# Kernel optimization log

Measured on AMD Instinct MI355X. Metric: run time of the kernel, lower is better.

Reference implementation:

```python
import jax, jax.numpy as jnp
import numpy as np
from jax import lax

# Hyperparameters from init_kwargs (inference/testing path of the RPN)
PRE_NMS = 6000        # pre_nms_top_n['testing']
POST_NMS = 1000       # post_nms_top_n['testing']
NMS_THRESH = 0.7
MIN_SIZE = 1.0
WX = WY = WW = WH = 1.0                      # reg_weights
BBOX_XFORM_CLIP = float(np.log(1000.0 / 16.0))  # standard BoxCoder clamp on dw/dh


def _decode(deltas, anchors):
    # deltas, anchors: [K, 4] -> decoded boxes [K, 4] (x1,y1,x2,y2)
    wa = anchors[:, 2] - anchors[:, 0]
    ha = anchors[:, 3] - anchors[:, 1]
    cxa = anchors[:, 0] + 0.5 * wa
    cya = anchors[:, 1] + 0.5 * ha
    dx = deltas[:, 0] / WX
    dy = deltas[:, 1] / WY
    dw = jnp.minimum(deltas[:, 2] / WW, BBOX_XFORM_CLIP)
    dh = jnp.minimum(deltas[:, 3] / WH, BBOX_XFORM_CLIP)
    cx = dx * wa + cxa
    cy = dy * ha + cya
    w = jnp.exp(dw) * wa
    h = jnp.exp(dh) * ha
    return jnp.stack([cx - 0.5 * w, cy - 0.5 * h, cx + 0.5 * w, cy + 0.5 * h], axis=-1)


def _nms_keep(boxes, valid, thresh):
    # Sequential NMS over score-sorted boxes [K,4]; 'valid' marks non-removed boxes.
    K = boxes.shape[0]
    x1, y1, x2, y2 = boxes[:, 0], boxes[:, 1], boxes[:, 2], boxes[:, 3]
    areas = (x2 - x1) * (y2 - y1)
    idxs = jnp.arange(K)

    def body(i, keep):
        xx1 = jnp.maximum(x1[i], x1)
        yy1 = jnp.maximum(y1[i], y1)
        xx2 = jnp.minimum(x2[i], x2)
        yy2 = jnp.minimum(y2[i], y2)
        inter = jnp.maximum(xx2 - xx1, 0.0) * jnp.maximum(yy2 - yy1, 0.0)
        iou = inter / (areas[i] + areas - inter + 1e-9)
        suppress = (iou > thresh) & (idxs > i)
        return jnp.where(keep[i], keep & ~suppress, keep)

    return lax.fori_loop(0, K, body, valid)


def _proposals_one(anchors, objectness, deltas, img_h, img_w):
    # anchors [N,4], objectness [N], deltas [N,4] -> proposals [POST_NMS, 4]
    k = min(objectness.shape[0], PRE_NMS)
    scores, idx = lax.top_k(objectness, k)          # topk filter (sorted desc)
    boxes = _decode(deltas[idx], anchors[idx])      # anchor decode on top-k only
    # process_box: clip to image, filter small boxes (masked, not removed, for jit)
    x1 = jnp.clip(boxes[:, 0], 0.0, img_w)
    y1 = jnp.clip(boxes[:, 1], 0.0, img_h)
    x2 = jnp.clip(boxes[:, 2], 0.0, img_w)
    y2 = jnp.clip(boxes[:, 3], 0.0, img_h)
    boxes = jnp.stack([x1, y1, x2, y2], axis=-1)
    valid = ((x2 - x1) >= MIN_SIZE) & ((y2 - y1) >= MIN_SIZE)
    keep = _nms_keep(boxes, valid, NMS_THRESH)
    # Compact kept boxes (score order) into a fixed [POST_NMS,4] buffer, zero-padded
    rank = jnp.cumsum(keep.astype(jnp.int32)) - 1
    tgt = jnp.where(keep & (rank < POST_NMS), rank, POST_NMS)  # POST_NMS -> dropped
    out = jnp.zeros((POST_NMS, 4), boxes.dtype).at[tgt].set(boxes, mode='drop')
    return out


def setup_inputs() -> dict:
    key = jax.random.key(0)
    k1, k2, k3, k4 = jax.random.split(key, 4)
    B, N = 8, 500000
    IMG = 1024
    # Valid anchor boxes: random centers in-image, sizes in [16, 256]
    cxy = jax.random.uniform(k1, (B, N, 2), jnp.float32, 0.0, float(IMG))
    wh = jax.random.uniform(k2, (B, N, 2), jnp.float32, 16.0, 256.0)
    anchors = jnp.concatenate([cxy - 0.5 * wh, cxy + 0.5 * wh], axis=-1)
    objectness = jax.random.normal(k3, (B, N), jnp.float32)
    pred_bbox_delta = 0.1 * jax.random.normal(k4, (B, N, 4), jnp.float32)
    return {"anchors": anchors, "objectness": objectness,
            "pred_bbox_delta": pred_bbox_delta, "img_h": IMG, "img_w": IMG}


def reference(anchors, objectness, pred_bbox_delta, img_h, img_w):
    h, w = float(img_h), float(img_w)
    f = jax.vmap(lambda a, o, d: _proposals_one(a, o, d, h, w))
    return f(anchors, objectness, pred_bbox_delta)  # [B, POST_NMS, 4]
```

## Files before the change

### kernel.cpp

```cpp
#include <hip/hip_runtime.h>
#include <cstdint>
#include <cmath>

#define NBATCH   8
#define NPB      500000
#define PRE_NMS  6000
#define POST_NMS 1000
#define NWORDS   94
#define NBINS    16384
#define CANDCAP  8192
#define BBOX_CLIP 4.135166556742356f
#define TI 16
#define TJ 512
#define WIN 16
#define CNT_PAD 64
#define SORT_CHUNK 2048

#define F_SORT 1u
#define F_COMP 2u
#define F_OOB  4u

__device__ __forceinline__ unsigned monot(float f) {
    unsigned b = __float_as_uint(f);
    return (b & 0x80000000u) ? ~b : (b | 0x80000000u);
}

__device__ __forceinline__ bool iou_gt_thr(float inter, float den) {
    const double MID = (double)0.7f + 0x1p-25;
    return (double)inter >= MID * (double)den;
}

__global__ __launch_bounds__(256) void hist_kernel(const float* __restrict__ obj,
                                                   unsigned* __restrict__ hist) {
    __shared__ unsigned lh[NBINS];
    const int b = blockIdx.y;
    for (int q = threadIdx.x; q < NBINS; q += 256) lh[q] = 0;
    __syncthreads();
    const float* p = obj + (size_t)b * NPB;
    const int stride = gridDim.x * 256;
    for (int i = blockIdx.x * 256 + threadIdx.x; i < NPB; i += stride) {
        unsigned u = monot(p[i]);
        atomicAdd(&lh[u >> 18], 1u);
    }
    __syncthreads();
    unsigned* gh = hist + (size_t)b * NBINS;
    for (int q = threadIdx.x; q < NBINS; q += 256) {
        unsigned v = lh[q];
        if (v) atomicAdd(&gh[q], v);
    }
}

__global__ __launch_bounds__(256) void thresh_kernel(const unsigned* __restrict__ hist,
                                                     unsigned* __restrict__ tbin) {
    __shared__ unsigned part[256], pre[256];
    const int b = blockIdx.x;
    const unsigned* gh = hist + (size_t)b * NBINS;
    const int t = threadIdx.x;
    const int PER = NBINS / 256;
    unsigned s = 0;
    for (int d = 0; d < PER; ++d) s += gh[NBINS - 1 - (t * PER + d)];
    part[t] = s;
    __syncthreads();
    if (t == 0) {
        unsigned run = 0;
        for (int q = 0; q < 256; ++q) { pre[q] = run; run += part[q]; }
    }
    __syncthreads();
    unsigned c = pre[t];
    if (c < PRE_NMS && c + part[t] >= PRE_NMS) {
        unsigned run = c;
        for (int d = 0; d < PER; ++d) {
            int bin = NBINS - 1 - (t * PER + d);
            run += gh[bin];
            if (run >= PRE_NMS) { tbin[b] = (unsigned)bin; break; }
        }
    }
}

__global__ __launch_bounds__(256) void compact_kernel(const float* __restrict__ obj,
                                                      const unsigned* __restrict__ tbin,
                                                      unsigned long long* __restrict__ cand,
                                                      unsigned* __restrict__ ccnt) {
    const int b = blockIdx.y;
    const unsigned T = tbin[b];
    const float* p = obj + (size_t)b * NPB;
    unsigned long long* cb = cand + (size_t)b * CANDCAP;
    const int lane = threadIdx.x & 63;
    const int stride = gridDim.x * 256;
    for (int i = blockIdx.x * 256 + threadIdx.x; i < NPB; i += stride) {
        unsigned u = monot(p[i]);
        const bool pred = (u >> 18) >= T;
        unsigned long long bal = __ballot(pred);
        if (bal == 0) continue;
        unsigned base = 0;
        if (lane == 0) base = atomicAdd(&ccnt[(size_t)b * CNT_PAD], __popcll(bal));
        base = (unsigned)__shfl((int)base, 0);
        if (pred) {
            unsigned pos = base + (unsigned)__popcll(bal & ((1ULL << lane) - 1ULL));
            if (pos < CANDCAP)
                cb[pos] = ((unsigned long long)u << 32) | (unsigned)(~i);
        }
    }
}

__global__ __launch_bounds__(512) void sort_local_kernel(unsigned long long* __restrict__ cand) {
    __shared__ unsigned long long s[SORT_CHUNK];
    const int blk = blockIdx.x;
    const int b = blk >> 2, c = blk & 3;
    unsigned long long* cb = cand + (size_t)b * CANDCAP + (size_t)c * SORT_CHUNK;
    const int t = threadIdx.x;
    for (int i = t; i < SORT_CHUNK; i += 512) s[i] = cb[i];
    __syncthreads();
    for (unsigned k = 2; k <= SORT_CHUNK; k <<= 1) {
        const bool kfull = (k == SORT_CHUNK);
        const bool upfull = (c & 1) == 0;
        for (unsigned j = k >> 1; j > 0; j >>= 1) {
            for (unsigned ii = t; ii < SORT_CHUNK; ii += 512) {
                unsigned l = ii ^ j;
                if (l > ii) {
                    unsigned long long a = s[ii], d = s[l];
                    bool up = kfull ? upfull : ((ii & k) == 0);
                    if (up ? (a < d) : (a > d)) { s[ii] = d; s[l] = a; }
                }
            }
            __syncthreads();
        }
    }
    for (int i = t; i < SORT_CHUNK; i += 512) cb[i] = s[i];
}

__global__ __launch_bounds__(1024) void sort_merge_kernel(const unsigned long long* __restrict__ cand,
                                                          const float* __restrict__ obj,
                                                          unsigned* __restrict__ topk,
                                                          unsigned* __restrict__ flags) {
    __shared__ unsigned long long s[CANDCAP];
    const int b = blockIdx.x, t = threadIdx.x;
    const unsigned long long* cb = cand + (size_t)b * CANDCAP;
    for (int i = t; i < CANDCAP; i += 1024) s[i] = cb[i];
    __syncthreads();
    for (unsigned k = 2 * SORT_CHUNK; k <= CANDCAP; k <<= 1) {
        for (unsigned j = k >> 1; j > 0; j >>= 1) {
            for (unsigned ii = t; ii < CANDCAP; ii += 1024) {
                unsigned l = ii ^ j;
                if (l > ii) {
                    unsigned long long a = s[ii], c = s[l];
                    bool up = (ii & k) == 0;
                    if (up ? (a < c) : (a > c)) { s[ii] = c; s[l] = a; }
                }
            }
            __syncthreads();
        }
    }
    unsigned f = 0;
    for (int r = t; r < PRE_NMS; r += 1024) {
        unsigned long long c = s[r];
        unsigned idx = ~(unsigned)(c & 0xffffffffULL);
        if (idx >= NPB) { f |= F_OOB; idx = 0; }
        else if (monot(obj[(size_t)b * NPB + idx]) != (unsigned)(c >> 32)) f |= F_COMP;
        if (r < PRE_NMS - 1 && !(c > s[r + 1])) f |= F_SORT;
        topk[(size_t)b * PRE_NMS + r] = idx;
    }
    if (f) atomicOr(&flags[b], f);
}

__global__ __launch_bounds__(256) void decode_kernel(const float* __restrict__ anchors,
                                                     const float* __restrict__ deltas,
                                                     const unsigned* __restrict__ topk,
                                                     const int* __restrict__ imh,
                                                     const int* __restrict__ imw,
                                                     float* __restrict__ boxes,
                                                     float* __restrict__ areas,
                                                     unsigned long long* __restrict__ validm) {
    const int b = blockIdx.y;
    const int r = blockIdx.x * 256 + threadIdx.x;
    const bool active = r < PRE_NMS;
    int vh = imh[0], vw = imw[0];
    float ih = (vh > 0 && vh < (1 << 20)) ? (float)vh : __int_as_float(vh);
    float iw = (vw > 0 && vw < (1 << 20)) ? (float)vw : __int_as_float(vw);
    bool valid = false;
    if (active) {
        unsigned idx = topk[(size_t)b * PRE_NMS + r];
        if (idx >= NPB) idx = 0;
        const float4 a = ((const float4*)anchors)[(size_t)b * NPB + idx];
        const float4 d = ((const float4*)deltas)[(size_t)b * NPB + idx];
        float wa = a.z - a.x, ha = a.w - a.y;
        float cxa = a.x + 0.5f * wa, cya = a.y + 0.5f * ha;
        float dw = fminf(d.z, BBOX_CLIP), dh = fminf(d.w, BBOX_CLIP);
        float cx = __fadd_rn(__fmul_rn(d.x, wa), cxa);
        float cy = __fadd_rn(__fmul_rn(d.y, ha), cya);
        float ew = (float)::exp((double)dw), eh = (float)::exp((double)dh);
        float w = __fmul_rn(ew, wa), h = __fmul_rn(eh, ha);
        float x1 = cx - 0.5f * w, y1 = cy - 0.5f * h;
        float x2 = cx + 0.5f * w, y2 = cy + 0.5f * h;
        x1 = fminf(fmaxf(x1, 0.f), iw); y1 = fminf(fmaxf(y1, 0.f), ih);
        x2 = fminf(fmaxf(x2, 0.f), iw); y2 = fminf(fmaxf(y2, 0.f), ih);
        valid = (x2 - x1 >= 1.0f) && (y2 - y1 >= 1.0f);
        ((float4*)boxes)[(size_t)b * PRE_NMS + r] = make_float4(x1, y1, x2, y2);
        areas[(size_t)b * PRE_NMS + r] = __fmul_rn(x2 - x1, y2 - y1);
    }
    unsigned long long bal = __ballot(valid);
    int w = r >> 6;
    if ((threadIdx.x & 63) == 0 && w < NWORDS) validm[(size_t)b * NWORDS + w] = bal;
}

__global__ __launch_bounds__(256) void mask_kernel(const float* __restrict__ boxes,
                                                   const float* __restrict__ areas,
                                                   unsigned long long* __restrict__ mask) {
    __shared__ float4 sb[TJ];
    __shared__ float  sa[TJ];
    const int b = blockIdx.x & 7;
    const int i0 = (blockIdx.x >> 3) * TI;
    const int jbase = (i0 >> 6) << 6;
    const int wv = threadIdx.x >> 6, ln = threadIdx.x & 63;
    const int ir = i0 + 4 * wv;
    float4 bx[4]; float ar[4]; int wlo[4];
    unsigned long long* rowp[4];
#pragma unroll
    for (int r = 0; r < 4; ++r) {
        const int i = ir + r;
        bx[r]   = ((const float4*)boxes)[(size_t)b * PRE_NMS + i];
        ar[r]   = areas[(size_t)b * PRE_NMS + i];
        rowp[r] = mask + ((size_t)b * PRE_NMS + i) * NWORDS;
        wlo[r]  = i >> 6;
    }
    for (int t0 = jbase; t0 < NWORDS * 64; t0 += TJ) {
        for (int e = threadIdx.x; e < TJ; e += 256) {
            int j = t0 + e;
            if (j < PRE_NMS) {
                sb[e] = ((const float4*)boxes)[(size_t)b * PRE_NMS + j];
                sa[e] = areas[(size_t)b * PRE_NMS + j];
            } else { sb[e] = make_float4(0.f, 0.f, 0.f, 0.f); sa[e] = 0.f; }
        }
        __syncthreads();
        for (int wl = 0; wl < TJ / 64; ++wl) {
            const int w = (t0 >> 6) + wl;
            if (w >= NWORDS) break;
            const int e = wl * 64 + ln;
            const int j = t0 + e;
            const float4 bj = sb[e];
            const float aj = sa[e];
            const bool jin = (j < PRE_NMS);
#pragma unroll
            for (int r = 0; r < 4; ++r) {
                float xx1 = fmaxf(bx[r].x, bj.x), yy1 = fmaxf(bx[r].y, bj.y);
                float xx2 = fminf(bx[r].z, bj.z), yy2 = fminf(bx[r].w, bj.w);
                float inter = __fmul_rn(fmaxf(__fsub_rn(xx2, xx1), 0.f),
                                        fmaxf(__fsub_rn(yy2, yy1), 0.f));
                float den = __fadd_rn(__fsub_rn(__fadd_rn(ar[r], aj), inter), 1e-9f);
                bool p = jin && (j > ir + r) && iou_gt_thr(inter, den);
                unsigned long long m = __ballot(p);
                if (ln == 0 && w >= wlo[r]) rowp[r][w] = m;
            }
        }
        __syncthreads();
    }
}

__global__ __launch_bounds__(64) void scan_kernel(const unsigned long long* __restrict__ mask,
                                                  const unsigned long long* __restrict__ validm,
                                                  const float* __restrict__ boxes,
                                                  const unsigned* __restrict__ flags,
                                                  const unsigned* __restrict__ ccnt,
                                                  float* __restrict__ out) {
    const int b = blockIdx.x, lane = threadIdx.x;
    const unsigned long long* mb = mask + (size_t)b * PRE_NMS * NWORDS;
    const int w0 = 2 * lane, w1 = 2 * lane + 1;
    unsigned long long r_lo = (w0 < NWORDS) ? ~validm[(size_t)b * NWORDS + w0] : ~0ULL;
    unsigned long long r_hi = (w1 < NWORDS) ? ~validm[(size_t)b * NWORDS + w1] : ~0ULL;
    int count = 0;

    uint4 MA[WIN], MB[WIN], MC[WIN];
    unsigned long long WA[WIN], WB[WIN], WC[WIN];
    float4 bxA, bxB, bxC;

#define ISSUE(M, W, BX, base_)                                                   \
    {                                                                            \
        const int bb_ = (base_);                                                 \
        const char* rb_ = (const char*)(mb + (size_t)bb_ * NWORDS);              \
        const int wI_ = bb_ >> 6;                                                \
        _Pragma("unroll")                                                        \
        for (int q = 0; q < WIN; ++q) {                                          \
            const char* rp_ = rb_ + (size_t)q * (NWORDS * 8);                    \
            M[q] = *(const uint4*)(rp_ + (size_t)lane * 16);                     \
            W[q] = *(const unsigned long long*)(rp_ + (size_t)wI_ * 8);          \
        }                                                                        \
        BX = (lane < WIN)                                                        \
                 ? ((const float4*)boxes)[(size_t)b * PRE_NMS + bb_ + lane]      \
                 : make_float4(0.f, 0.f, 0.f, 0.f);                              \
    }

#define RESOLVE(M, W, BX, base_)                                                 \
    {                                                                            \
        const int bb_ = (base_);                                                 \
        const int wR_ = bb_ >> 6, s0_ = bb_ & 63;                                \
        const unsigned long long sel_ = (wR_ & 1) ? r_hi : r_lo;                 \
        const int srcl_ = wR_ >> 1;                                              \
        const unsigned lo_ = (unsigned)__shfl((int)(unsigned)(sel_ & 0xffffffffULL), srcl_); \
        const unsigned hi_ = (unsigned)__shfl((int)(unsigned)(sel_ >> 32), srcl_);           \
        const unsigned long long ww_ = ((unsigned long long)hi_ << 32) | lo_;    \
        unsigned cand_ = (unsigned)((~ww_) >> s0_) & 0xFFFFu;                    \
        unsigned kept_ = 0;                                                      \
        const int cb_ = count;                                                   \
        _Pragma("unroll")                                                        \
        for (int q = 0; q < WIN; ++q) {                                          \
            if (((cand_ >> q) & 1u) && count < POST_NMS) {                       \
                kept_ |= 1u << q; ++count;                                       \
                cand_ &= ~(unsigned)(W[q] >> s0_);                               \
            }                                                                    \
        }                                                                        \
        const bool v0_ = (w0 >= wR_), v1_ = (w1 >= wR_);                         \
        _Pragma("unroll")                                                        \
        for (int q = 0; q < WIN; ++q) {                                          \
            if (kept_ & (1u << q)) {                                             \
                const uint4 m_ = M[q];                                           \
                if (v0_) r_lo |= ((unsigned long long)m_.y << 32) | m_.x;        \
                if (v1_) r_hi |= ((unsigned long long)m_.w << 32) | m_.z;        \
            }                                                                    \
        }                                                                        \
        if (lane < WIN && (kept_ & (1u << lane))) {                              \
            const int rank_ = cb_ + __popc(kept_ & ((1u << lane) - 1u));         \
            ((float4*)out)[(size_t)b * POST_NMS + rank_] = BX;                   \
        }                                                                        \
    }

    ISSUE(MA, WA, bxA, 0)
    ISSUE(MB, WB, bxB, WIN)
    bool done = false;
    for (int base = 0; base < PRE_NMS && !done; base += 3 * WIN) {
        const int n2 = base + 2 * WIN;
        ISSUE(MC, WC, bxC, (n2 < PRE_NMS) ? n2 : 0)
        RESOLVE(MA, WA, bxA, base)
        done = (count >= POST_NMS);
        if (!done) {
            const int n3 = base + 3 * WIN;
            ISSUE(MA, WA, bxA, (n3 < PRE_NMS) ? n3 : 0)
            RESOLVE(MB, WB, bxB, base + WIN)
            done = (count >= POST_NMS);
        }
        if (!done) {
            const int n4 = base + 4 * WIN;
            ISSUE(MB, WB, bxB, (n4 < PRE_NMS) ? n4 : 0)
            RESOLVE(MC, WC, bxC, base + 2 * WIN)
            done = (count >= POST_NMS);
        }
    }
#undef ISSUE
#undef RESOLVE

    if (lane == 0) {
        float canary = 0.f;
        const unsigned cc = ccnt[(size_t)b * CNT_PAD];
        const unsigned fl = flags[b];
        if (cc > CANDCAP)       canary = 111000.f;
        else if (cc < PRE_NMS)  canary = 222000.f;
        if (fl & F_SORT)        canary = 333000.f;
        if (fl & F_COMP)        canary = 444000.f;
        if (fl & F_OOB)         canary = 777000.f;
        if (canary != 0.f) out[(size_t)b * POST_NMS * 4] = canary;
    }
}

extern "C" void kernel_launch(void* const* d_in, const int* in_sizes, int n_in,
                              void* d_out, int out_size, void* d_ws, size_t ws_size,
                              hipStream_t stream) {
    const float* anchors = (const float*)d_in[0];
    const float* obj     = (const float*)d_in[1];
    const float* deltas  = (const float*)d_in[2];
    const int*   imh     = (const int*)d_in[3];
    const int*   imw     = (const int*)d_in[4];
    float* out = (float*)d_out;
    char* ws = (char*)d_ws;

    size_t off = 0;
    auto alloc = [&](size_t bytes) {
        size_t o = off;
        off = (off + bytes + 511) & ~(size_t)511;
        return o;
    };
    const size_t HIST  = alloc((size_t)NBATCH * NBINS * 4);
    const size_t TBIN  = alloc((size_t)NBATCH * 4);
    const size_t CCNT  = alloc((size_t)NBATCH * CNT_PAD * 4);
    const size_t FLAGS = alloc((size_t)NBATCH * 4);
    const size_t CAND  = alloc((size_t)NBATCH * CANDCAP * 8);
    const size_t ZEND  = off;
    const size_t TOPK  = alloc((size_t)NBATCH * PRE_NMS * 4);
    const size_t BOX   = alloc((size_t)NBATCH * PRE_NMS * 16);
    const size_t AREA  = alloc((size_t)NBATCH * PRE_NMS * 4);
    const size_t VALID = alloc((size_t)NBATCH * NWORDS * 8);
    const size_t MASK  = alloc((size_t)NBATCH * PRE_NMS * NWORDS * 8);
    (void)alloc(1024);
    if (ws_size < off) return;

    unsigned*            hist   = (unsigned*)(ws + HIST);
    unsigned*            tbin   = (unsigned*)(ws + TBIN);
    unsigned*            ccnt   = (unsigned*)(ws + CCNT);
    unsigned*            flags  = (unsigned*)(ws + FLAGS);
    unsigned long long*  cand   = (unsigned long long*)(ws + CAND);
    unsigned*            topk   = (unsigned*)(ws + TOPK);
    float*               boxes  = (float*)(ws + BOX);
    float*               areas  = (float*)(ws + AREA);
    unsigned long long*  validm = (unsigned long long*)(ws + VALID);
    unsigned long long*  maskp  = (unsigned long long*)(ws + MASK);

    hipMemsetAsync(ws, 0, ZEND, stream);
    hipMemsetAsync(out, 0, (size_t)out_size * sizeof(float), stream);

    hist_kernel      <<<dim3(32, NBATCH), 256, 0, stream>>>(obj, hist);
    thresh_kernel    <<<dim3(NBATCH), 256, 0, stream>>>(hist, tbin);
    compact_kernel   <<<dim3(128, NBATCH), 256, 0, stream>>>(obj, tbin, cand, ccnt);
    sort_local_kernel<<<dim3(NBATCH * (CANDCAP / SORT_CHUNK)), 512, 0, stream>>>(cand);
    sort_merge_kernel<<<dim3(NBATCH), 1024, 0, stream>>>(cand, obj, topk, flags);
    decode_kernel    <<<dim3((PRE_NMS + 255) / 256, NBATCH), 256, 0, stream>>>(
        anchors, deltas, topk, imh, imw, boxes, areas, validm);
    mask_kernel      <<<dim3((PRE_NMS / TI) * NBATCH), 256, 0, stream>>>(boxes, areas, maskp);
    scan_kernel      <<<dim3(NBATCH), 64, 0, stream>>>(maskp, validm, boxes, flags, ccnt, out);
    (void)in_sizes; (void)n_in; (void)ws_size;
}
```

Baseline: 379.2 us.

## Fuse box decode into sort merge and add contiguous diagonal mask array

Box decoding, clipping, area computation and the valid-bit ballot move into sort_merge_kernel, which removes the separate decode launch and the topk index buffer. The mask kernel drops its per-element bounds and upper-triangle tests, applying the triangle cut with a bit mask on the diagonal word only. It also writes each row's diagonal word into a separate contiguous diag array. The sequential scan kernel then reads diagonal words contiguously instead of with an NWORDS stride. In exchange, decode now runs on only 8 blocks, one per batch, which may serialise the anchor and delta gathers.

```diff
diff --git a/kernel.cpp b/kernel.cpp
--- a/kernel.cpp
+++ b/kernel.cpp
@@ -131,7 +131,13 @@
 
 __global__ __launch_bounds__(1024) void sort_merge_kernel(const unsigned long long* __restrict__ cand,
                                                           const float* __restrict__ obj,
-                                                          unsigned* __restrict__ topk,
+                                                          const float* __restrict__ anchors,
+                                                          const float* __restrict__ deltas,
+                                                          const int* __restrict__ imh,
+                                                          const int* __restrict__ imw,
+                                                          float* __restrict__ boxes,
+                                                          float* __restrict__ areas,
+                                                          unsigned long long* __restrict__ validm,
                                                           unsigned* __restrict__ flags) {
     __shared__ unsigned long long s[CANDCAP];
     const int b = blockIdx.x, t = threadIdx.x;
@@ -151,6 +157,9 @@
             __syncthreads();
         }
     }
+    int vh = imh[0], vw = imw[0];
+    float ih = (vh > 0 && vh < (1 << 20)) ? (float)vh : __int_as_float(vh);
+    float iw = (vw > 0 && vw < (1 << 20)) ? (float)vw : __int_as_float(vw);
     unsigned f = 0;
     for (int r = t; r < PRE_NMS; r += 1024) {
         unsigned long long c = s[r];
@@ -158,29 +167,6 @@
         if (idx >= NPB) { f |= F_OOB; idx = 0; }
         else if (monot(obj[(size_t)b * NPB + idx]) != (unsigned)(c >> 32)) f |= F_COMP;
         if (r < PRE_NMS - 1 && !(c > s[r + 1])) f |= F_SORT;
-        topk[(size_t)b * PRE_NMS + r] = idx;
-    }
-    if (f) atomicOr(&flags[b], f);
-}
-
-__global__ __launch_bounds__(256) void decode_kernel(const float* __restrict__ anchors,
-                                                     const float* __restrict__ deltas,
-                                                     const unsigned* __restrict__ topk,
-                                                     const int* __restrict__ imh,
-                                                     const int* __restrict__ imw,
-                                                     float* __restrict__ boxes,
-                                                     float* __restrict__ areas,
-                                                     unsigned long long* __restrict__ validm) {
-    const int b = blockIdx.y;
-    const int r = blockIdx.x * 256 + threadIdx.x;
-    const bool active = r < PRE_NMS;
-    int vh = imh[0], vw = imw[0];
-    float ih = (vh > 0 && vh < (1 << 20)) ? (float)vh : __int_as_float(vh);
-    float iw = (vw > 0 && vw < (1 << 20)) ? (float)vw : __int_as_float(vw);
-    bool valid = false;
-    if (active) {
-        unsigned idx = topk[(size_t)b * PRE_NMS + r];
-        if (idx >= NPB) idx = 0;
         const float4 a = ((const float4*)anchors)[(size_t)b * NPB + idx];
         const float4 d = ((const float4*)deltas)[(size_t)b * NPB + idx];
         float wa = a.z - a.x, ha = a.w - a.y;
@@ -194,18 +180,19 @@
         float x2 = cx + 0.5f * w, y2 = cy + 0.5f * h;
         x1 = fminf(fmaxf(x1, 0.f), iw); y1 = fminf(fmaxf(y1, 0.f), ih);
         x2 = fminf(fmaxf(x2, 0.f), iw); y2 = fminf(fmaxf(y2, 0.f), ih);
-        valid = (x2 - x1 >= 1.0f) && (y2 - y1 >= 1.0f);
+        bool valid = (x2 - x1 >= 1.0f) && (y2 - y1 >= 1.0f);
         ((float4*)boxes)[(size_t)b * PRE_NMS + r] = make_float4(x1, y1, x2, y2);
         areas[(size_t)b * PRE_NMS + r] = __fmul_rn(x2 - x1, y2 - y1);
-    }
-    unsigned long long bal = __ballot(valid);
-    int w = r >> 6;
-    if ((threadIdx.x & 63) == 0 && w < NWORDS) validm[(size_t)b * NWORDS + w] = bal;
+        unsigned long long bal = __ballot(valid);
+        if ((threadIdx.x & 63) == 0) validm[(size_t)b * NWORDS + (r >> 6)] = bal;
+    }
+    if (f) atomicOr(&flags[b], f);
 }
 
 __global__ __launch_bounds__(256) void mask_kernel(const float* __restrict__ boxes,
                                                    const float* __restrict__ areas,
-                                                   unsigned long long* __restrict__ mask) {
+                                                   unsigned long long* __restrict__ mask,
+                                                   unsigned long long* __restrict__ diag) {
     __shared__ float4 sb[TJ];
     __shared__ float  sa[TJ];
     const int b = blockIdx.x & 7;
@@ -213,6 +200,7 @@
     const int jbase = (i0 >> 6) << 6;
     const int wv = threadIdx.x >> 6, ln = threadIdx.x & 63;
     const int ir = i0 + 4 * wv;
+    unsigned long long* dgp = diag + (size_t)b * PRE_NMS;
     float4 bx[4]; float ar[4]; int wlo[4];
     unsigned long long* rowp[4];
 #pragma unroll
@@ -236,10 +224,8 @@
             const int w = (t0 >> 6) + wl;
             if (w >= NWORDS) break;
             const int e = wl * 64 + ln;
-            const int j = t0 + e;
             const float4 bj = sb[e];
             const float aj = sa[e];
-            const bool jin = (j < PRE_NMS);
 #pragma unroll
             for (int r = 0; r < 4; ++r) {
                 float xx1 = fmaxf(bx[r].x, bj.x), yy1 = fmaxf(bx[r].y, bj.y);
@@ -247,9 +233,17 @@
                 float inter = __fmul_rn(fmaxf(__fsub_rn(xx2, xx1), 0.f),
                                         fmaxf(__fsub_rn(yy2, yy1), 0.f));
                 float den = __fadd_rn(__fsub_rn(__fadd_rn(ar[r], aj), inter), 1e-9f);
-                bool p = jin && (j > ir + r) && iou_gt_thr(inter, den);
+                bool p = iou_gt_thr(inter, den);
                 unsigned long long m = __ballot(p);
-                if (ln == 0 && w >= wlo[r]) rowp[r][w] = m;
+                if (ln == 0) {
+                    if (w == wlo[r]) {
+                        m &= ~((2ULL << ((ir + r) & 63)) - 1ULL);
+                        rowp[r][w] = m;
+                        dgp[ir + r] = m;
+                    } else if (w > wlo[r]) {
+                        rowp[r][w] = m;
+                    }
+                }
             }
         }
         __syncthreads();
@@ -257,6 +251,7 @@
 }
 
 __global__ __launch_bounds__(64) void scan_kernel(const unsigned long long* __restrict__ mask,
+                                                  const unsigned long long* __restrict__ diag,
                                                   const unsigned long long* __restrict__ validm,
                                                   const float* __restrict__ boxes,
                                                   const unsigned* __restrict__ flags,
@@ -264,6 +259,7 @@
                                                   float* __restrict__ out) {
     const int b = blockIdx.x, lane = threadIdx.x;
     const unsigned long long* mb = mask + (size_t)b * PRE_NMS * NWORDS;
+    const unsigned long long* dg = diag + (size_t)b * PRE_NMS;
     const int w0 = 2 * lane, w1 = 2 * lane + 1;
     unsigned long long r_lo = (w0 < NWORDS) ? ~validm[(size_t)b * NWORDS + w0] : ~0ULL;
     unsigned long long r_hi = (w1 < NWORDS) ? ~validm[(size_t)b * NWORDS + w1] : ~0ULL;
@@ -277,12 +273,12 @@
     {                                                                            \
         const int bb_ = (base_);                                                 \
         const char* rb_ = (const char*)(mb + (size_t)bb_ * NWORDS);              \
-        const int wI_ = bb_ >> 6;                                                \
+        const unsigned long long* dgp_ = dg + bb_;   \
         _Pragma("unroll")                                                        \
         for (int q = 0; q < WIN; ++q) {                                          \
-            const char* rp_ = rb_ + (size_t)q * (NWORDS * 8);                    \
-            M[q] = *(const uint4*)(rp_ + (size_t)lane * 16);                     \
-            W[q] = *(const unsigned long long*)(rp_ + (size_t)wI_ * 8);          \
+            M[q] = *(const uint4*)(rb_ + (size_t)q * (NWORDS * 8)                \
+                                       + (size_t)lane * 16);                     \
+            W[q] = dgp_[q];                                                      \
         }                                                                        \
         BX = (lane < WIN)                                                        \
                  ? ((const float4*)boxes)[(size_t)b * PRE_NMS + bb_ + lane]      \
@@ -383,10 +379,10 @@
     const size_t FLAGS = alloc((size_t)NBATCH * 4);
     const size_t CAND  = alloc((size_t)NBATCH * CANDCAP * 8);
     const size_t ZEND  = off;
-    const size_t TOPK  = alloc((size_t)NBATCH * PRE_NMS * 4);
     const size_t BOX   = alloc((size_t)NBATCH * PRE_NMS * 16);
     const size_t AREA  = alloc((size_t)NBATCH * PRE_NMS * 4);
     const size_t VALID = alloc((size_t)NBATCH * NWORDS * 8);
+    const size_t DIAG  = alloc((size_t)NBATCH * PRE_NMS * 8);
     const size_t MASK  = alloc((size_t)NBATCH * PRE_NMS * NWORDS * 8);
     (void)alloc(1024);
     if (ws_size < off) return;
@@ -396,10 +392,10 @@
     unsigned*            ccnt   = (unsigned*)(ws + CCNT);
     unsigned*            flags  = (unsigned*)(ws + FLAGS);
     unsigned long long*  cand   = (unsigned long long*)(ws + CAND);
-    unsigned*            topk   = (unsigned*)(ws + TOPK);
     float*               boxes  = (float*)(ws + BOX);
     float*               areas  = (float*)(ws + AREA);
     unsigned long long*  validm = (unsigned long long*)(ws + VALID);
+    unsigned long long*  diag   = (unsigned long long*)(ws + DIAG);
     unsigned long long*  maskp  = (unsigned long long*)(ws + MASK);
 
     hipMemsetAsync(ws, 0, ZEND, stream);
@@ -409,10 +405,11 @@
     thresh_kernel    <<<dim3(NBATCH), 256, 0, stream>>>(hist, tbin);
     compact_kernel   <<<dim3(128, NBATCH), 256, 0, stream>>>(obj, tbin, cand, ccnt);
     sort_local_kernel<<<dim3(NBATCH * (CANDCAP / SORT_CHUNK)), 512, 0, stream>>>(cand);
-    sort_merge_kernel<<<dim3(NBATCH), 1024, 0, stream>>>(cand, obj, topk, flags);
-    decode_kernel    <<<dim3((PRE_NMS + 255) / 256, NBATCH), 256, 0, stream>>>(
-        anchors, deltas, topk, imh, imw, boxes, areas, validm);
-    mask_kernel      <<<dim3((PRE_NMS / TI) * NBATCH), 256, 0, stream>>>(boxes, areas, maskp);
-    scan_kernel      <<<dim3(NBATCH), 64, 0, stream>>>(maskp, validm, boxes, flags, ccnt, out);
+    sort_merge_kernel<<<dim3(NBATCH), 1024, 0, stream>>>(
+        cand, obj, anchors, deltas, imh, imw, boxes, areas, validm, flags);
+    mask_kernel      <<<dim3((PRE_NMS / TI) * NBATCH), 256, 0, stream>>>(
+        boxes, areas, maskp, diag);
+    scan_kernel      <<<dim3(NBATCH), 64, 0, stream>>>(
+        maskp, diag, validm, boxes, flags, ccnt, out);
     (void)in_sizes; (void)n_in; (void)ws_size;
 }
```

Measured after the change: 391.0 us. 3.1% more time.
